# Performance work log

Measured on AMD Instinct MI355X. Metric: run time of the kernel, lower is better.

The kernel has to match this reference:

```python
import jax, jax.numpy as jnp
import numpy as np
import math

P, DD, N, E, NDRUGS = 256, 128, 1024, 250000, 200000
BASELINE = 6.0

def _prelu(x, a):
    return jnp.where(x >= 0, x, a * x)

def _lrelu(x):
    return jnp.where(x >= 0, x, 0.2 * x)

def _lin(x, W, b):
    return x @ W.T + b

def setup_inputs() -> dict:
    key = jax.random.key(0)
    ks = jax.random.split(key, 40)
    f32 = jnp.float32
    inp = {}
    inp["target_features"] = jax.random.normal(ks[0], (P,), f32)
    inp["form_features"] = jax.random.normal(ks[1], (N, P), f32)
    inp["role_features"] = jax.random.normal(ks[2], (N, P), f32)
    inp["form_neighbors"] = jnp.arange(N, dtype=jnp.int32)
    inp["form_binds_src"] = jax.random.randint(ks[3], (E,), 0, N, jnp.int32)
    inp["form_binds_dst"] = jax.random.randint(ks[4], (E,), 0, NDRUGS, jnp.int32)
    inp["form_binds_y"] = jax.random.uniform(ks[5], (E,), f32, 4.0, 9.0)
    inp["role_neighbors"] = jnp.arange(N, dtype=jnp.int32)
    inp["role_binds_src"] = jax.random.randint(ks[6], (E,), 0, N, jnp.int32)
    inp["role_binds_dst"] = jax.random.randint(ks[7], (E,), 0, NDRUGS, jnp.int32)
    inp["role_binds_y"] = jax.random.uniform(ks[8], (E,), f32, 4.0, 9.0)
    inp["drug_features"] = jax.random.normal(ks[9], (NDRUGS, DD), f32)
    s = 0.02
    # prot_refiner: Linear(P,P) -> PReLU -> Linear(P,P)
    inp["Wr1"] = jax.random.normal(ks[10], (P, P), f32) * s
    inp["br1"] = jnp.zeros((P,), f32)
    inp["ar1"] = jnp.asarray(0.25, f32)
    inp["Wr2"] = jax.random.normal(ks[11], (P, P), f32) * s
    inp["br2"] = jnp.zeros((P,), f32)
    # q/k/v projections
    inp["Wq"] = jax.random.normal(ks[12], (DD, P), f32) * s
    inp["bq"] = jnp.zeros((DD,), f32)
    inp["Wk"] = jax.random.normal(ks[13], (DD, DD), f32) * s
    inp["bk"] = jnp.zeros((DD,), f32)
    inp["Wv"] = jax.random.normal(ks[14], (DD, DD), f32) * s
    inp["bv"] = jnp.zeros((DD,), f32)
    inp["layer_emb"] = jax.random.normal(ks[15], (2, 16), f32) * s
    # attn_net: (2P+16)->128->64->1 with LeakyReLU(0.2)
    inp["Wa1"] = jax.random.normal(ks[16], (128, 2 * P + 16), f32) * s
    inp["ba1"] = jnp.zeros((128,), f32)
    inp["Wa2"] = jax.random.normal(ks[17], (64, 128), f32) * s
    inp["ba2"] = jnp.zeros((64,), f32)
    inp["Wa3"] = jax.random.normal(ks[18], (1, 64), f32) * s
    inp["ba3"] = jnp.zeros((1,), f32)
    # integration_mlp: Linear(DD,P) -> PReLU -> Linear(P,P)
    inp["Wi1"] = jax.random.normal(ks[19], (P, DD), f32) * s
    inp["bi1"] = jnp.zeros((P,), f32)
    inp["ai"] = jnp.asarray(0.25, f32)
    inp["Wi2"] = jax.random.normal(ks[20], (P, P), f32) * s
    inp["bi2"] = jnp.zeros((P,), f32)
    inp["ln_g"] = jnp.ones((P,), f32)
    inp["ln_b"] = jnp.zeros((P,), f32)
    return inp

def reference(target_features, form_features, role_features, form_neighbors,
              form_binds_src, form_binds_dst, form_binds_y,
              role_neighbors, role_binds_src, role_binds_dst, role_binds_y,
              drug_features,
              Wr1, br1, ar1, Wr2, br2, Wq, bq, Wk, bk, Wv, bv, layer_emb,
              Wa1, ba1, Wa2, ba2, Wa3, ba3, Wi1, bi1, ai, Wi2, bi2, ln_g, ln_b):
    def refine(x):
        return _lin(_prelu(_lin(x, Wr1, br1), ar1), Wr2, br2)

    zt = refine(target_features)          # [P]
    zf = refine(form_features)            # [N, P]
    zr = refine(role_features)            # [N, P]
    Qv = _lin(zt, Wq, bq)                 # [DD]

    def build_msgs(neighbors, src, dst, y):
        # segment id for each edge: position of src in (sorted) neighbor_ids;
        # edges whose src is not a neighbor go to the dummy segment n.
        n = neighbors.shape[0]
        pos = jnp.clip(jnp.searchsorted(neighbors, src), 0, n - 1)
        seg = jnp.where(neighbors[pos] == src, pos, n)
        d = drug_features[dst]                                # [E, DD] gather
        K = _lin(d, Wk, bk)                                   # [E, DD]
        V = _lin(d, Wv, bv) * (y - BASELINE)[:, None]         # [E, DD]
        s = (K @ Qv) / math.sqrt(DD)                          # [E]
        nseg = n + 1
        m = jax.ops.segment_max(s, seg, num_segments=nseg)    # per-neighbor max
        ex = jnp.exp(s - m[seg])                              # stable softmax numerator
        den = jax.ops.segment_sum(ex, seg, num_segments=nseg)[:n]          # [N]
        num = jax.ops.segment_sum(ex[:, None] * V, seg, num_segments=nseg)[:n]  # [N, DD]
        return jnp.where(den[:, None] > 0, num / jnp.maximum(den, 1e-30)[:, None], 0.0)

    form_msgs = build_msgs(form_neighbors, form_binds_src, form_binds_dst, form_binds_y)
    role_msgs = build_msgs(role_neighbors, role_binds_src, role_binds_dst, role_binds_y)

    def attn(zn, layer_id):
        n = zn.shape[0]
        le = jnp.broadcast_to(layer_emb[layer_id], (n, 16))
        zt_e = jnp.broadcast_to(zt, (n, P))
        x = jnp.concatenate([zt_e, zn, le], axis=-1)          # [N, 2P+16]
        h = _lrelu(_lin(x, Wa1, ba1))
        h = _lrelu(_lin(h, Wa2, ba2))
        return _lin(h, Wa3, ba3)                              # [N, 1]

    all_msgs = jnp.concatenate([form_msgs, role_msgs], axis=0)   # [2N, DD]
    all_attn = jnp.concatenate([attn(zf, 0), attn(zr, 1)], axis=0)  # [2N, 1]
    w = jax.nn.softmax(all_attn, axis=0)
    v_prior = jnp.sum(w * all_msgs, axis=0)                   # [DD]
    integ = _lin(_prelu(_lin(v_prior, Wi1, bi1), ai), Wi2, bi2)
    x = zt + integ
    mu = jnp.mean(x, axis=-1, keepdims=True)
    var = jnp.var(x, axis=-1, keepdims=True)
    z = (x - mu) / jnp.sqrt(var + 1e-5) * ln_g + ln_b
    return (z, form_msgs, role_msgs)
```

## Files before the change

kernel.cpp:

```cpp
#include <hip/hip_runtime.h>

#define NP 256
#define NDD 128
#define NN 1024
#define NE 250000
#define SB 62
#define RB2 257

__global__ __launch_bounds__(256) void prep_kernel(
    const float* __restrict__ Wr1, const float* __restrict__ Wr2,
    const float* __restrict__ Wa1, const float* __restrict__ Wa2,
    const float* __restrict__ Wv,
    float* __restrict__ Wr1T, float* __restrict__ Wr2T,
    float* __restrict__ Wa1mT, float* __restrict__ Wa2T, float* __restrict__ WvT)
{
  __shared__ float T[64][65];
  int b = blockIdx.x, t = threadIdx.x;
  const float* src; float* dst;
  int sC, sr0, sc0, dC, dr0, dc0;
  if (b < 16){        int ti=b;    src=Wr1; sC=256; sr0=(ti/4)*64; sc0=(ti%4)*64;
                      dst=Wr1T; dC=256; dr0=sc0; dc0=sr0; }
  else if (b < 32){   int ti=b-16; src=Wr2; sC=256; sr0=(ti/4)*64; sc0=(ti%4)*64;
                      dst=Wr2T; dC=256; dr0=sc0; dc0=sr0; }
  else if (b < 40){   int ti=b-32; src=Wa1; sC=528; sr0=(ti/4)*64; sc0=256+(ti%4)*64;
                      dst=Wa1mT; dC=128; dr0=(ti%4)*64; dc0=sr0; }
  else if (b < 42){   int ti=b-40; src=Wa2; sC=128; sr0=0; sc0=ti*64;
                      dst=Wa2T; dC=64; dr0=sc0; dc0=0; }
  else {              int ti=b-42; src=Wv;  sC=128; sr0=(ti/2)*64; sc0=(ti%2)*64;
                      dst=WvT; dC=128; dr0=sc0; dc0=sr0; }
  #pragma unroll
  for (int j = 0; j < 16; j++){
    int idx = t + j*256;
    int r = idx >> 6, c = idx & 63;
    T[c][r] = src[(size_t)(sr0 + r)*sC + sc0 + c];
  }
  __syncthreads();
  #pragma unroll
  for (int j = 0; j < 16; j++){
    int idx = t + j*256;
    int r = idx >> 6, c = idx & 63;
    dst[(size_t)(dr0 + r)*dC + dc0 + c] = T[r][c];
  }
}

__global__ __launch_bounds__(256) void refine_qk_hist_kernel(
    const float* __restrict__ tgt, const float* __restrict__ formf, const float* __restrict__ rolef,
    const float* __restrict__ Wr1T, const float* __restrict__ br1, const float* __restrict__ ar1,
    const float* __restrict__ Wr2T, const float* __restrict__ br2,
    const float* __restrict__ Wq, const float* __restrict__ bq,
    const float* __restrict__ Wk, const float* __restrict__ bk,
    const float* __restrict__ Wa1, const float* __restrict__ ba1, const float* __restrict__ lemb,
    const int* __restrict__ neighF, const int* __restrict__ srcF,
    const int* __restrict__ neighR, const int* __restrict__ srcR,
    float* __restrict__ zt, float* __restrict__ zf, float* __restrict__ zr,
    float* __restrict__ qk, float* __restrict__ s0, float* __restrict__ cl,
    int* __restrict__ count)
{
  __shared__ float X[8][NP];
  __shared__ float H[8][NP];
  __shared__ float Zs[NP];
  __shared__ float Q[NDD];
  __shared__ float red[NDD];
  const int t = threadIdx.x;

  if (blockIdx.x >= RB2){
    int bi = blockIdx.x - RB2;
    int role = bi >= SB ? 1 : 0;
    int blk = bi - role*SB;
    const int* neigh = role ? neighR : neighF;
    const int* src   = role ? srcR   : srcF;
    int* cnt = count + role*NN;
    int* NB = (int*)&X[0][0];
    int* lh = NB + NN;
    #pragma unroll
    for (int i = 0; i < NN/256; i++){
      NB[t + i*256] = neigh[t + i*256];
      lh[t + i*256] = 0;
    }
    __syncthreads();
    #pragma unroll
    for (int i = 0; i < 16; i++){
      int e = blk*4096 + i*256 + t;
      if (e < NE){
        int s = src[e];
        int pos;
        if ((unsigned)s < NN && NB[s] == s) pos = s;
        else {
          int lo = 0, hi = NN;
          while (lo < hi){ int mid = (lo+hi)>>1; if (NB[mid] < s) lo = mid+1; else hi = mid; }
          pos = lo < NN ? lo : NN-1;
        }
        if (NB[pos] == s) atomicAdd(&lh[pos], 1);
      }
    }
    __syncthreads();
    #pragma unroll
    for (int i = 0; i < NN/256; i++){
      int c = lh[t + i*256];
      if (c > 0) atomicAdd(&cnt[t + i*256], c);
    }
    return;
  }

  const int base = blockIdx.x * 8;
  #pragma unroll
  for (int r = 0; r < 8; r++){
    int row = base + r;
    if (row < 2*NN + 1){
      const float* xp;
      if (row == 0)        xp = tgt;
      else if (row <= NN)  xp = formf + (size_t)(row-1)*NP;
      else                 xp = rolef + (size_t)(row-NN-1)*NP;
      X[r][t] = xp[t];
    } else {
      X[r][t] = 0.f;
    }
  }
  __syncthreads();
  const float a1 = ar1[0];
  float acc[8];
  #pragma unroll
  for (int r = 0; r < 8; r++) acc[r] = 0.f;
  for (int k = 0; k < NP; k += 4){
    float w0 = Wr1T[(k+0)*NP + t];
    float w1 = Wr1T[(k+1)*NP + t];
    float w2 = Wr1T[(k+2)*NP + t];
    float w3 = Wr1T[(k+3)*NP + t];
    #pragma unroll
    for (int r = 0; r < 8; r++){
      float4 x = *reinterpret_cast<const float4*>(&X[r][k]);
      acc[r] = fmaf(w0, x.x, acc[r]);
      acc[r] = fmaf(w1, x.y, acc[r]);
      acc[r] = fmaf(w2, x.z, acc[r]);
      acc[r] = fmaf(w3, x.w, acc[r]);
    }
  }
  const float b1 = br1[t];
  #pragma unroll
  for (int r = 0; r < 8; r++){
    float h = acc[r] + b1;
    H[r][t] = h >= 0.f ? h : a1*h;
  }
  __syncthreads();
  #pragma unroll
  for (int r = 0; r < 8; r++) acc[r] = 0.f;
  for (int k = 0; k < NP; k += 4){
    float w0 = Wr2T[(k+0)*NP + t];
    float w1 = Wr2T[(k+1)*NP + t];
    float w2 = Wr2T[(k+2)*NP + t];
    float w3 = Wr2T[(k+3)*NP + t];
    #pragma unroll
    for (int r = 0; r < 8; r++){
      float4 h4 = *reinterpret_cast<const float4*>(&H[r][k]);
      acc[r] = fmaf(w0, h4.x, acc[r]);
      acc[r] = fmaf(w1, h4.y, acc[r]);
      acc[r] = fmaf(w2, h4.z, acc[r]);
      acc[r] = fmaf(w3, h4.w, acc[r]);
    }
  }
  const float b2 = br2[t];
  #pragma unroll
  for (int r = 0; r < 8; r++){
    int row = base + r;
    if (row < 2*NN + 1){
      float v = acc[r] + b2;
      float* op;
      if (row == 0){ op = zt; Zs[t] = v; }
      else if (row <= NN)  op = zf + (size_t)(row-1)*NP;
      else                 op = zr + (size_t)(row-NN-1)*NP;
      op[t] = v;
    }
  }

  if (blockIdx.x == 0){
    __syncthreads();
    if (t < NDD){
      float a = 0.f;
      const float4* wq = reinterpret_cast<const float4*>(Wq) + t*(NP/4);
      for (int k4 = 0; k4 < NP/4; k4++){
        float4 w = wq[k4];
        float4 zv = *reinterpret_cast<const float4*>(&Zs[k4*4]);
        a = fmaf(w.x, zv.x, fmaf(w.y, zv.y, fmaf(w.z, zv.z, fmaf(w.w, zv.w, a))));
      }
      float qv = a + bq[t];
      Q[t] = qv;
      red[t] = bk[t] * qv;
    }
    __syncthreads();
    const float rs = 0.08838834764831845f;
    if (t < NDD){
      float a2 = 0.f;
      for (int j = 0; j < NDD; j++) a2 = fmaf(Wk[j*NDD + t], Q[j], a2);
      qk[t] = a2 * rs;
    }
    for (int o = 64; o; o >>= 1){
      if (t < o) red[t] += red[t+o];
      __syncthreads();
    }
    if (t == 0) s0[0] = red[0] * rs;
    {
      int l = t >> 7, tt = t & 127;
      const float4* wrow = reinterpret_cast<const float4*>(Wa1 + (size_t)tt*528);
      float a = 0.f;
      for (int k4 = 0; k4 < 64; k4++){
        float4 w = wrow[k4];
        float4 zv = *reinterpret_cast<const float4*>(&Zs[k4*4]);
        a = fmaf(w.x, zv.x, fmaf(w.y, zv.y, fmaf(w.z, zv.z, fmaf(w.w, zv.w, a))));
      }
      const float* wle = Wa1 + (size_t)tt*528 + 512;
      const float* le = lemb + l*16;
      #pragma unroll
      for (int j = 0; j < 16; j++) a = fmaf(wle[j], le[j], a);
      cl[l*NDD + tt] = a + ba1[tt];
    }
  }
}

__device__ __forceinline__ int seg_of(const int* NB, int s){
  if ((unsigned)s < NN && NB[s] == s) return s;
  int lo = 0, hi = NN;
  while (lo < hi){ int mid = (lo+hi)>>1; if (NB[mid] < s) lo = mid+1; else hi = mid; }
  return lo < NN ? lo : NN-1;
}

__global__ __launch_bounds__(1024) void scatter_kernel(
    const int* __restrict__ neighF, const int* __restrict__ srcF,
    const int* __restrict__ dstF, const float* __restrict__ yF,
    const int* __restrict__ neighR, const int* __restrict__ srcR,
    const int* __restrict__ dstR, const float* __restrict__ yR,
    const int* __restrict__ count, int* __restrict__ cursor0,
    int* __restrict__ offsets, int2* __restrict__ edges)
{
  __shared__ int NB[NN];
  __shared__ int lcur[NN];
  __shared__ int sscan[NN];
  __shared__ int obase[NN];
  __shared__ int lbase[NN];
  int bi = blockIdx.x;
  int role = bi >= SB ? 1 : 0;
  int blk = bi - role*SB;
  const int* neigh = role ? neighR : neighF;
  const int* src   = role ? srcR   : srcF;
  const int* dst   = role ? dstR   : dstF;
  const float* yb  = role ? yR     : yF;
  int* cur0 = cursor0 + role*NN;
  int2* ed  = edges   + (size_t)role*NE;
  int t = threadIdx.x;
  NB[t] = neigh[t];
  lcur[t] = 0;
  int c0 = count[role*NN + t];
  sscan[t] = c0;
  __syncthreads();
  for (int o = 1; o < NN; o <<= 1){
    int v = (t >= o) ? sscan[t-o] : 0;
    __syncthreads();
    sscan[t] += v;
    __syncthreads();
  }
  obase[t] = sscan[t] - c0;
  if (blk == 0) offsets[role*NN + t] = sscan[t] - c0;
  __syncthreads();

  int segr[4], locr[4]; int2 edr[4];
  #pragma unroll
  for (int i = 0; i < 4; i++){
    int e = blk*4096 + i*1024 + t;
    segr[i] = -1;
    if (e < NE){
      int s = src[e];
      int pos = seg_of(NB, s);
      if (NB[pos] == s){
        segr[i] = pos;
        edr[i]  = make_int2(dst[e], __float_as_int(yb[e]));
        locr[i] = atomicAdd(&lcur[pos], 1);
      }
    }
  }
  __syncthreads();
  int c = lcur[t];
  if (c > 0) lbase[t] = obase[t] + atomicAdd(&cur0[t], c);
  __syncthreads();
  #pragma unroll
  for (int i = 0; i < 4; i++){
    if (segr[i] >= 0){
      ed[(size_t)(lbase[segr[i]] + locr[i])] = edr[i];
    }
  }
}

__global__ __launch_bounds__(256) void seg_kernel(
    const float* __restrict__ drug,
    const int2* __restrict__ edges,
    const int* __restrict__ offsets, const int* __restrict__ count,
    const float* __restrict__ qk, const float* __restrict__ s0p,
    float* __restrict__ g, float* __restrict__ den, float* __restrict__ cfac)
{
  int b = blockIdx.x;
  int tid = threadIdx.x;
  int w = tid >> 6, lane = tid & 63, l32 = lane & 31, half = lane >> 5;
  int off = offsets[b], cnt = count[b];
  int l = b >> 10;
  const int2* eb = edges + (size_t)l*NE;
  float4 q = reinterpret_cast<const float4*>(qk)[l32];
  float s0 = s0p[0];
  int chunk = (cnt + 3) >> 2;
  int start = w*chunk;
  int end = min(start + chunk, cnt);
  float dn = 0.f, cc = 0.f;
  float4 ga = make_float4(0.f,0.f,0.f,0.f);
  for (int i = start; i < end; i += 8){
    int dstp[4]; float yp[4]; bool vp[4];
    #pragma unroll
    for (int p2 = 0; p2 < 4; p2++){
      int idx = i + 2*p2 + half;
      bool v = idx < end;
      int2 e = eb[off + (v ? idx : start)];
      dstp[p2] = e.x; yp[p2] = __int_as_float(e.y); vp[p2] = v;
    }
    float4 dv[4];
    #pragma unroll
    for (int p2 = 0; p2 < 4; p2++){
      dv[p2] = reinterpret_cast<const float4*>(drug + (size_t)dstp[p2]*NDD)[l32];
    }
    #pragma unroll
    for (int p2 = 0; p2 < 4; p2++){
      float4 d = dv[p2];
      float s = fmaf(d.x, q.x, fmaf(d.y, q.y, fmaf(d.z, q.z, d.w*q.w)));
      s += __shfl_xor(s, 16, 64);
      s += __shfl_xor(s,  8, 64);
      s += __shfl_xor(s,  4, 64);
      s += __shfl_xor(s,  2, 64);
      s += __shfl_xor(s,  1, 64);
      float ex = vp[p2] ? __expf(s + s0) : 0.f;
      float wv = ex * (yp[p2] - 6.0f);
      dn += ex; cc += wv;
      ga.x = fmaf(wv, d.x, ga.x);
      ga.y = fmaf(wv, d.y, ga.y);
      ga.z = fmaf(wv, d.z, ga.z);
      ga.w = fmaf(wv, d.w, ga.w);
    }
  }
  __shared__ float4 sG[8][32];
  __shared__ float sD[8], sC[8];
  int slot = w*2 + half;
  sG[slot][l32] = ga;
  if (l32 == 0){ sD[slot] = dn; sC[slot] = cc; }
  __syncthreads();
  if (tid < NDD){
    int a = tid >> 2, c = tid & 3;
    float v = 0.f;
    #pragma unroll
    for (int k = 0; k < 8; k++)
      v += reinterpret_cast<const float*>(&sG[k][a])[c];
    g[(size_t)b*NDD + tid] = v;
    if (tid == 0){
      float ds = 0.f, cs = 0.f;
      #pragma unroll
      for (int k = 0; k < 8; k++){ ds += sD[k]; cs += sC[k]; }
      den[b] = ds; cfac[b] = cs;
    }
  }
}

__global__ __launch_bounds__(256) void attn_msgs_kernel(
    const float* __restrict__ zf, const float* __restrict__ zr,
    const float* __restrict__ cl,
    const float* __restrict__ Wa1mT,
    const float* __restrict__ Wa2T, const float* __restrict__ ba2,
    const float* __restrict__ Wa3, const float* __restrict__ ba3,
    const float* __restrict__ g, const float* __restrict__ den, const float* __restrict__ cfac,
    const float* __restrict__ WvT, const float* __restrict__ bv,
    float* __restrict__ attn, float* __restrict__ msgsf, float* __restrict__ outm)
{
  int t = threadIdx.x;
  int tt = t & 127, grp = t >> 7;
  if (blockIdx.x < 256){
    __shared__ float Zn[8][NP];
    __shared__ float H1[8][NDD];
    int base = blockIdx.x*8;
    int layer = blockIdx.x >> 7;
    const float* zsrc = layer ? zr : zf;
    #pragma unroll
    for (int r = 0; r < 8; r++){
      int nn = (base + r) & (NN-1);
      Zn[r][t] = zsrc[(size_t)nn*NP + t];
    }
    __syncthreads();
    float acc[4];
    #pragma unroll
    for (int r = 0; r < 4; r++) acc[r] = 0.f;
    for (int k = 0; k < NP; k += 4){
      float w0 = Wa1mT[(k+0)*NDD + tt];
      float w1 = Wa1mT[(k+1)*NDD + tt];
      float w2 = Wa1mT[(k+2)*NDD + tt];
      float w3 = Wa1mT[(k+3)*NDD + tt];
      #pragma unroll
      for (int r = 0; r < 4; r++){
        float4 x = *reinterpret_cast<const float4*>(&Zn[grp*4 + r][k]);
        acc[r] = fmaf(w0, x.x, acc[r]);
        acc[r] = fmaf(w1, x.y, acc[r]);
        acc[r] = fmaf(w2, x.z, acc[r]);
        acc[r] = fmaf(w3, x.w, acc[r]);
      }
    }
    float c1 = cl[layer*NDD + tt];
    #pragma unroll
    for (int r = 0; r < 4; r++){
      float h = acc[r] + c1;
      H1[grp*4 + r][tt] = h >= 0.f ? h : 0.2f*h;
    }
    __syncthreads();
    if (t < 64){
      float acc2[8];
      #pragma unroll
      for (int r = 0; r < 8; r++) acc2[r] = 0.f;
      for (int k = 0; k < NDD; k += 4){
        float w0 = Wa2T[(k+0)*64 + t];
        float w1 = Wa2T[(k+1)*64 + t];
        float w2 = Wa2T[(k+2)*64 + t];
        float w3 = Wa2T[(k+3)*64 + t];
        #pragma unroll
        for (int r = 0; r < 8; r++){
          float4 h4 = *reinterpret_cast<const float4*>(&H1[r][k]);
          acc2[r] = fmaf(w0, h4.x, acc2[r]);
          acc2[r] = fmaf(w1, h4.y, acc2[r]);
          acc2[r] = fmaf(w2, h4.z, acc2[r]);
          acc2[r] = fmaf(w3, h4.w, acc2[r]);
        }
      }
      float b2 = ba2[t];
      float w3v = Wa3[t];
      float b3 = ba3[0];
      #pragma unroll
      for (int r = 0; r < 8; r++){
        float h = acc2[r] + b2;
        h = h >= 0.f ? h : 0.2f*h;
        float p = w3v * h;
        #pragma unroll
        for (int o = 32; o; o >>= 1) p += __shfl_xor(p, o, 64);
        if (t == 0) attn[base + r] = p + b3;
      }
    }
  } else {
    __shared__ float G[8][NDD];
    int base = (blockIdx.x - 256)*8;
    #pragma unroll
    for (int r = 0; r < 4; r++) G[grp*4 + r][tt] = g[(size_t)(base + grp*4 + r)*NDD + tt];
    __syncthreads();
    float acc[4];
    #pragma unroll
    for (int r = 0; r < 4; r++) acc[r] = 0.f;
    for (int k = 0; k < NDD; k += 4){
      float w0 = WvT[(k+0)*NDD + tt];
      float w1 = WvT[(k+1)*NDD + tt];
      float w2 = WvT[(k+2)*NDD + tt];
      float w3 = WvT[(k+3)*NDD + tt];
      #pragma unroll
      for (int r = 0; r < 4; r++){
        float4 gv = *reinterpret_cast<const float4*>(&G[grp*4 + r][k]);
        acc[r] = fmaf(w0, gv.x, acc[r]);
        acc[r] = fmaf(w1, gv.y, acc[r]);
        acc[r] = fmaf(w2, gv.z, acc[r]);
        acc[r] = fmaf(w3, gv.w, acc[r]);
      }
    }
    float bvj = bv[tt];
    #pragma unroll
    for (int r = 0; r < 4; r++){
      int row = base + grp*4 + r;
      float dn = den[row];
      float v = 0.f;
      if (dn > 0.f) v = (acc[r] + bvj*cfac[row]) / fmaxf(dn, 1e-30f);
      msgsf[(size_t)row*NDD + tt] = v;
      outm [(size_t)row*NDD + tt] = v;
    }
  }
}

__global__ __launch_bounds__(1024) void vprior_final_kernel(
    const float* __restrict__ attn, const float* __restrict__ msgsf,
    const float* __restrict__ zt,
    const float* __restrict__ Wi1, const float* __restrict__ bi1, const float* __restrict__ ai,
    const float* __restrict__ Wi2, const float* __restrict__ bi2,
    const float* __restrict__ ln_g, const float* __restrict__ ln_b,
    float* __restrict__ zout)
{
  __shared__ float A[2*NN];
  __shared__ float red[1024];
  __shared__ float Pp[8][NDD];
  __shared__ float V[NDD];
  __shared__ float T1[NP];
  __shared__ float red2[NP];
  int t = threadIdx.x;
  A[t] = attn[t]; A[t+1024] = attn[t+1024];
  __syncthreads();
  float mx = fmaxf(A[t], A[t+1024]);
  red[t] = mx; __syncthreads();
  for (int o = 512; o; o >>= 1){ if (t < o) red[t] = fmaxf(red[t], red[t+o]); __syncthreads(); }
  float M = red[0]; __syncthreads();
  float sm = __expf(A[t] - M) + __expf(A[t+1024] - M);
  red[t] = sm; __syncthreads();
  for (int o = 512; o; o >>= 1){ if (t < o) red[t] += red[t+o]; __syncthreads(); }
  float inv = 1.f / red[0]; __syncthreads();
  A[t]      = __expf(A[t]      - M) * inv;
  A[t+1024] = __expf(A[t+1024] - M) * inv;
  __syncthreads();
  int j = t & 127, grp = t >> 7;
  float acc = 0.f;
  int i0 = grp * 256;
  for (int i = i0; i < i0 + 256; i++) acc = fmaf(A[i], msgsf[(size_t)i*NDD + j], acc);
  Pp[grp][j] = acc;
  __syncthreads();
  if (t < NDD){
    float v = 0.f;
    #pragma unroll
    for (int gg = 0; gg < 8; gg++) v += Pp[gg][t];
    V[t] = v;
  }
  __syncthreads();
  float x = 0.f;
  if (t < NP){
    float a1 = 0.f;
    const float4* w1 = reinterpret_cast<const float4*>(Wi1) + t*(NDD/4);
    for (int k4 = 0; k4 < NDD/4; k4++){
      float4 w = w1[k4];
      float4 vv = *reinterpret_cast<const float4*>(&V[k4*4]);
      a1 = fmaf(w.x, vv.x, fmaf(w.y, vv.y, fmaf(w.z, vv.z, fmaf(w.w, vv.w, a1))));
    }
    float h = a1 + bi1[t];
    float a = ai[0];
    T1[t] = h >= 0.f ? h : a*h;
  }
  __syncthreads();
  if (t < NP){
    float a2 = 0.f;
    const float4* w2 = reinterpret_cast<const float4*>(Wi2) + t*(NP/4);
    for (int k4 = 0; k4 < NP/4; k4++){
      float4 w = w2[k4];
      float4 hv = *reinterpret_cast<const float4*>(&T1[k4*4]);
      a2 = fmaf(w.x, hv.x, fmaf(w.y, hv.y, fmaf(w.z, hv.z, fmaf(w.w, hv.w, a2))));
    }
    x = zt[t] + a2 + bi2[t];
    red2[t] = x;
  }
  __syncthreads();
  for (int o = 128; o; o >>= 1){ if (t < o) red2[t] += red2[t+o]; __syncthreads(); }
  float mu = red2[0] * (1.f/256.f); __syncthreads();
  float d = x - mu;
  if (t < NP) red2[t] = d*d;
  __syncthreads();
  for (int o = 128; o; o >>= 1){ if (t < o) red2[t] += red2[t+o]; __syncthreads(); }
  if (t < NP){
    float var = red2[0] * (1.f/256.f);
    float zz = d * rsqrtf(var + 1e-5f) * ln_g[t] + ln_b[t];
    zout[t] = zz;
  }
}

extern "C" void kernel_launch(void* const* d_in, const int* in_sizes, int n_in,
                              void* d_out, int out_size, void* d_ws, size_t ws_size,
                              hipStream_t stream)
{
  const float* tgt    = (const float*)d_in[0];
  const float* formf  = (const float*)d_in[1];
  const float* rolef  = (const float*)d_in[2];
  const int* fneigh   = (const int*)d_in[3];
  const int* fsrc     = (const int*)d_in[4];
  const int* fdst     = (const int*)d_in[5];
  const float* fy     = (const float*)d_in[6];
  const int* rneigh   = (const int*)d_in[7];
  const int* rsrc     = (const int*)d_in[8];
  const int* rdst     = (const int*)d_in[9];
  const float* ry     = (const float*)d_in[10];
  const float* drug   = (const float*)d_in[11];
  const float* Wr1 = (const float*)d_in[12];
  const float* br1 = (const float*)d_in[13];
  const float* ar1 = (const float*)d_in[14];
  const float* Wr2 = (const float*)d_in[15];
  const float* br2 = (const float*)d_in[16];
  const float* Wq  = (const float*)d_in[17];
  const float* bq  = (const float*)d_in[18];
  const float* Wk  = (const float*)d_in[19];
  const float* bk  = (const float*)d_in[20];
  const float* Wv  = (const float*)d_in[21];
  const float* bv  = (const float*)d_in[22];
  const float* lemb= (const float*)d_in[23];
  const float* Wa1 = (const float*)d_in[24];
  const float* ba1 = (const float*)d_in[25];
  const float* Wa2 = (const float*)d_in[26];
  const float* ba2 = (const float*)d_in[27];
  const float* Wa3 = (const float*)d_in[28];
  const float* ba3 = (const float*)d_in[29];
  const float* Wi1 = (const float*)d_in[30];
  const float* bi1 = (const float*)d_in[31];
  const float* ai  = (const float*)d_in[32];
  const float* Wi2 = (const float*)d_in[33];
  const float* bi2 = (const float*)d_in[34];
  const float* lng = (const float*)d_in[35];
  const float* lnb = (const float*)d_in[36];
  (void)in_sizes; (void)n_in; (void)out_size; (void)ws_size;

  float* ws = (float*)d_ws;
  float* zt_     = ws + 0;
  float* zf_     = ws + 256;
  float* zr_     = ws + 262400;
  float* qk_     = ws + 524544;
  float* s0_     = ws + 524672;
  float* cl_     = ws + 524800;
  float* attn_   = ws + 525056;
  float* den_    = ws + 527104;
  float* cfac_   = ws + 529152;
  float* g_      = ws + 531200;
  float* msgsf_  = ws + 793344;
  int*   count_  = (int*)(ws + 1055488);
  int*   offs_   = (int*)(ws + 1057536);
  int*   cursor_ = (int*)(ws + 1059584);
  int2*  edges_  = (int2*)(ws + 1061632);
  float* Wr1T_   = ws + 3061632;
  float* Wr2T_   = ws + 3127168;
  float* Wa1mT_  = ws + 3192704;
  float* Wa2T_   = ws + 3225472;
  float* WvT_    = ws + 3233664;

  hipMemsetAsync(count_, 0, 3*2*NN*sizeof(int), stream);

  prep_kernel<<<46, 256, 0, stream>>>(Wr1, Wr2, Wa1, Wa2, Wv,
                                      Wr1T_, Wr2T_, Wa1mT_, Wa2T_, WvT_);

  refine_qk_hist_kernel<<<RB2 + 2*SB, 256, 0, stream>>>(
      tgt, formf, rolef, Wr1T_, br1, ar1, Wr2T_, br2, Wq, bq, Wk, bk,
      Wa1, ba1, lemb,
      fneigh, fsrc, rneigh, rsrc,
      zt_, zf_, zr_, qk_, s0_, cl_, count_);

  scatter_kernel<<<2*SB, 1024, 0, stream>>>(fneigh, fsrc, fdst, fy,
                                            rneigh, rsrc, rdst, ry,
                                            count_, cursor_, offs_, edges_);

  seg_kernel<<<2*NN, 256, 0, stream>>>(drug, edges_, offs_, count_, qk_, s0_,
                                       g_, den_, cfac_);

  attn_msgs_kernel<<<512, 256, 0, stream>>>(zf_, zr_, cl_,
                                            Wa1mT_, Wa2T_, ba2, Wa3, ba3,
                                            g_, den_, cfac_, WvT_, bv,
                                            attn_, msgsf_, (float*)d_out + NP);
  vprior_final_kernel<<<1, 1024, 0, stream>>>(attn_, msgsf_, zt_,
                                              Wi1, bi1, ai, Wi2, bi2,
                                              lng, lnb, (float*)d_out);
}
```

Measured before the change: 367.4 us.

## Fuse attention MLP into refine kernel and Wv projection into segment kernel

Moves the target-row refine and the q/k/cl computation into an extra block of the prep kernel. The neighbor refine kernel now runs the attention MLP straight on its refined rows, so zf/zr never go to global memory. The Wv projection is folded into the segment kernel, which drops the g/den/cfac round trip and removes the attn_msgs kernel launch. In exchange the refine blocks do more serial work and each segment block runs a small per-row matvec, and launch bounds of 4 waves/SIMD are added that may limit registers.

```diff
diff --git a/kernel.cpp b/kernel.cpp
--- a/kernel.cpp
+++ b/kernel.cpp
@@ -5,17 +5,95 @@
 #define NN 1024
 #define NE 250000
 #define SB 62
-#define RB2 257
+#define RB 256
 
 __global__ __launch_bounds__(256) void prep_kernel(
     const float* __restrict__ Wr1, const float* __restrict__ Wr2,
     const float* __restrict__ Wa1, const float* __restrict__ Wa2,
     const float* __restrict__ Wv,
+    const float* __restrict__ tgt, const float* __restrict__ br1,
+    const float* __restrict__ ar1, const float* __restrict__ br2,
+    const float* __restrict__ Wq, const float* __restrict__ bq,
+    const float* __restrict__ Wk, const float* __restrict__ bk,
+    const float* __restrict__ ba1, const float* __restrict__ lemb,
     float* __restrict__ Wr1T, float* __restrict__ Wr2T,
-    float* __restrict__ Wa1mT, float* __restrict__ Wa2T, float* __restrict__ WvT)
+    float* __restrict__ Wa1mT, float* __restrict__ Wa2T, float* __restrict__ WvT,
+    float* __restrict__ zt, float* __restrict__ qk, float* __restrict__ s0,
+    float* __restrict__ cl)
 {
+  int b = blockIdx.x, t = threadIdx.x;
+  if (b == 46){
+    __shared__ float Xs[NP], Hs[NP], Zs[NP], Q[NDD], red[NDD];
+    Xs[t] = tgt[t];
+    __syncthreads();
+    float a = 0.f;
+    {
+      const float4* w1 = reinterpret_cast<const float4*>(Wr1) + (size_t)t*(NP/4);
+      for (int k4 = 0; k4 < NP/4; k4++){
+        float4 w = w1[k4];
+        float4 x = *reinterpret_cast<const float4*>(&Xs[k4*4]);
+        a = fmaf(w.x,x.x,fmaf(w.y,x.y,fmaf(w.z,x.z,fmaf(w.w,x.w,a))));
+      }
+    }
+    float h = a + br1[t];
+    float a1 = ar1[0];
+    Hs[t] = h >= 0.f ? h : a1*h;
+    __syncthreads();
+    a = 0.f;
+    {
+      const float4* w2 = reinterpret_cast<const float4*>(Wr2) + (size_t)t*(NP/4);
+      for (int k4 = 0; k4 < NP/4; k4++){
+        float4 w = w2[k4];
+        float4 x = *reinterpret_cast<const float4*>(&Hs[k4*4]);
+        a = fmaf(w.x,x.x,fmaf(w.y,x.y,fmaf(w.z,x.z,fmaf(w.w,x.w,a))));
+      }
+    }
+    float zv = a + br2[t];
+    Zs[t] = zv;
+    zt[t] = zv;
+    __syncthreads();
+    if (t < NDD){
+      float aq = 0.f;
+      const float4* wq = reinterpret_cast<const float4*>(Wq) + (size_t)t*(NP/4);
+      for (int k4 = 0; k4 < NP/4; k4++){
+        float4 w = wq[k4];
+        float4 x = *reinterpret_cast<const float4*>(&Zs[k4*4]);
+        aq = fmaf(w.x,x.x,fmaf(w.y,x.y,fmaf(w.z,x.z,fmaf(w.w,x.w,aq))));
+      }
+      float qv = aq + bq[t];
+      Q[t] = qv;
+      red[t] = bk[t]*qv;
+    }
+    __syncthreads();
+    const float rs = 0.08838834764831845f;
+    if (t < NDD){
+      float a2 = 0.f;
+      for (int j = 0; j < NDD; j++) a2 = fmaf(Wk[j*NDD + t], Q[j], a2);
+      qk[t] = a2 * rs;
+    }
+    for (int o = 64; o; o >>= 1){
+      if (t < o) red[t] += red[t+o];
+      __syncthreads();
+    }
+    if (t == 0) s0[0] = red[0]*rs;
+    {
+      int l = t >> 7, tt = t & 127;
+      const float4* wrow = reinterpret_cast<const float4*>(Wa1 + (size_t)tt*528);
+      float ac = 0.f;
+      for (int k4 = 0; k4 < 64; k4++){
+        float4 w = wrow[k4];
+        float4 x = *reinterpret_cast<const float4*>(&Zs[k4*4]);
+        ac = fmaf(w.x,x.x,fmaf(w.y,x.y,fmaf(w.z,x.z,fmaf(w.w,x.w,ac))));
+      }
+      const float* wle = Wa1 + (size_t)tt*528 + 512;
+      const float* le = lemb + l*16;
+      #pragma unroll
+      for (int j2 = 0; j2 < 16; j2++) ac = fmaf(wle[j2], le[j2], ac);
+      cl[l*NDD + tt] = ac + ba1[tt];
+    }
+    return;
+  }
   __shared__ float T[64][65];
-  int b = blockIdx.x, t = threadIdx.x;
   const float* src; float* dst;
   int sC, sr0, sc0, dC, dr0, dc0;
   if (b < 16){        int ti=b;    src=Wr1; sC=256; sr0=(ti/4)*64; sc0=(ti%4)*64;
@@ -43,28 +121,24 @@
   }
 }
 
-__global__ __launch_bounds__(256) void refine_qk_hist_kernel(
-    const float* __restrict__ tgt, const float* __restrict__ formf, const float* __restrict__ rolef,
+__global__ __launch_bounds__(256, 4) void refine_attn_hist_kernel(
+    const float* __restrict__ formf, const float* __restrict__ rolef,
     const float* __restrict__ Wr1T, const float* __restrict__ br1, const float* __restrict__ ar1,
     const float* __restrict__ Wr2T, const float* __restrict__ br2,
-    const float* __restrict__ Wq, const float* __restrict__ bq,
-    const float* __restrict__ Wk, const float* __restrict__ bk,
-    const float* __restrict__ Wa1, const float* __restrict__ ba1, const float* __restrict__ lemb,
+    const float* __restrict__ cl, const float* __restrict__ Wa1mT,
+    const float* __restrict__ Wa2T, const float* __restrict__ ba2,
+    const float* __restrict__ Wa3, const float* __restrict__ ba3,
     const int* __restrict__ neighF, const int* __restrict__ srcF,
     const int* __restrict__ neighR, const int* __restrict__ srcR,
-    float* __restrict__ zt, float* __restrict__ zf, float* __restrict__ zr,
-    float* __restrict__ qk, float* __restrict__ s0, float* __restrict__ cl,
-    int* __restrict__ count)
+    float* __restrict__ attn, int* __restrict__ count)
 {
   __shared__ float X[8][NP];
   __shared__ float H[8][NP];
-  __shared__ float Zs[NP];
-  __shared__ float Q[NDD];
-  __shared__ float red[NDD];
+  __shared__ float H1[8][NDD];
   const int t = threadIdx.x;
 
-  if (blockIdx.x >= RB2){
-    int bi = blockIdx.x - RB2;
+  if (blockIdx.x >= RB){
+    int bi = blockIdx.x - RB;
     int role = bi >= SB ? 1 : 0;
     int blk = bi - role*SB;
     const int* neigh = role ? neighR : neighF;
@@ -102,19 +176,13 @@
     return;
   }
 
-  const int base = blockIdx.x * 8;
+  const int abase = blockIdx.x * 8;
+  const int layer = blockIdx.x >> 7;
+  const float* fsrcp = layer ? rolef : formf;
   #pragma unroll
   for (int r = 0; r < 8; r++){
-    int row = base + r;
-    if (row < 2*NN + 1){
-      const float* xp;
-      if (row == 0)        xp = tgt;
-      else if (row <= NN)  xp = formf + (size_t)(row-1)*NP;
-      else                 xp = rolef + (size_t)(row-NN-1)*NP;
-      X[r][t] = xp[t];
-    } else {
-      X[r][t] = 0.f;
-    }
+    int nn = (abase + r) & (NN-1);
+    X[r][t] = fsrcp[(size_t)nn*NP + t];
   }
   __syncthreads();
   const float a1 = ar1[0];
@@ -160,58 +228,63 @@
   }
   const float b2 = br2[t];
   #pragma unroll
-  for (int r = 0; r < 8; r++){
-    int row = base + r;
-    if (row < 2*NN + 1){
-      float v = acc[r] + b2;
-      float* op;
-      if (row == 0){ op = zt; Zs[t] = v; }
-      else if (row <= NN)  op = zf + (size_t)(row-1)*NP;
-      else                 op = zr + (size_t)(row-NN-1)*NP;
-      op[t] = v;
-    }
-  }
-
-  if (blockIdx.x == 0){
-    __syncthreads();
-    if (t < NDD){
-      float a = 0.f;
-      const float4* wq = reinterpret_cast<const float4*>(Wq) + t*(NP/4);
-      for (int k4 = 0; k4 < NP/4; k4++){
-        float4 w = wq[k4];
-        float4 zv = *reinterpret_cast<const float4*>(&Zs[k4*4]);
-        a = fmaf(w.x, zv.x, fmaf(w.y, zv.y, fmaf(w.z, zv.z, fmaf(w.w, zv.w, a))));
+  for (int r = 0; r < 8; r++) X[r][t] = acc[r] + b2;
+  __syncthreads();
+
+  const int tt = t & 127, grp = t >> 7;
+  const float c1 = cl[layer*NDD + tt];
+  float acc2[4];
+  #pragma unroll
+  for (int r = 0; r < 4; r++) acc2[r] = 0.f;
+  for (int k = 0; k < NP; k += 4){
+    float w0 = Wa1mT[(k+0)*NDD + tt];
+    float w1 = Wa1mT[(k+1)*NDD + tt];
+    float w2 = Wa1mT[(k+2)*NDD + tt];
+    float w3 = Wa1mT[(k+3)*NDD + tt];
+    #pragma unroll
+    for (int r = 0; r < 4; r++){
+      float4 x = *reinterpret_cast<const float4*>(&X[grp*4 + r][k]);
+      acc2[r] = fmaf(w0, x.x, acc2[r]);
+      acc2[r] = fmaf(w1, x.y, acc2[r]);
+      acc2[r] = fmaf(w2, x.z, acc2[r]);
+      acc2[r] = fmaf(w3, x.w, acc2[r]);
+    }
+  }
+  #pragma unroll
+  for (int r = 0; r < 4; r++){
+    float h = acc2[r] + c1;
+    H1[grp*4 + r][tt] = h >= 0.f ? h : 0.2f*h;
+  }
+  __syncthreads();
+  if (t < 64){
+    float a2r[8];
+    #pragma unroll
+    for (int r = 0; r < 8; r++) a2r[r] = 0.f;
+    for (int k = 0; k < NDD; k += 4){
+      float w0 = Wa2T[(k+0)*64 + t];
+      float w1 = Wa2T[(k+1)*64 + t];
+      float w2 = Wa2T[(k+2)*64 + t];
+      float w3 = Wa2T[(k+3)*64 + t];
+      #pragma unroll
+      for (int r = 0; r < 8; r++){
+        float4 h4 = *reinterpret_cast<const float4*>(&H1[r][k]);
+        a2r[r] = fmaf(w0, h4.x, a2r[r]);
+        a2r[r] = fmaf(w1, h4.y, a2r[r]);
+        a2r[r] = fmaf(w2, h4.z, a2r[r]);
+        a2r[r] = fmaf(w3, h4.w, a2r[r]);
       }
-      float qv = a + bq[t];
-      Q[t] = qv;
-      red[t] = bk[t] * qv;
-    }
-    __syncthreads();
-    const float rs = 0.08838834764831845f;
-    if (t < NDD){
-      float a2 = 0.f;
-      for (int j = 0; j < NDD; j++) a2 = fmaf(Wk[j*NDD + t], Q[j], a2);
-      qk[t] = a2 * rs;
-    }
-    for (int o = 64; o; o >>= 1){
-      if (t < o) red[t] += red[t+o];
-      __syncthreads();
-    }
-    if (t == 0) s0[0] = red[0] * rs;
-    {
-      int l = t >> 7, tt = t & 127;
-      const float4* wrow = reinterpret_cast<const float4*>(Wa1 + (size_t)tt*528);
-      float a = 0.f;
-      for (int k4 = 0; k4 < 64; k4++){
-        float4 w = wrow[k4];
-        float4 zv = *reinterpret_cast<const float4*>(&Zs[k4*4]);
-        a = fmaf(w.x, zv.x, fmaf(w.y, zv.y, fmaf(w.z, zv.z, fmaf(w.w, zv.w, a))));
-      }
-      const float* wle = Wa1 + (size_t)tt*528 + 512;
-      const float* le = lemb + l*16;
+    }
+    float b2a = ba2[t];
+    float w3v = Wa3[t];
+    float b3 = ba3[0];
+    #pragma unroll
+    for (int r = 0; r < 8; r++){
+      float h = a2r[r] + b2a;
+      h = h >= 0.f ? h : 0.2f*h;
+      float p = w3v * h;
       #pragma unroll
-      for (int j = 0; j < 16; j++) a = fmaf(wle[j], le[j], a);
-      cl[l*NDD + tt] = a + ba1[tt];
+      for (int o = 32; o; o >>= 1) p += __shfl_xor(p, o, 64);
+      if (t == 0) attn[abase + r] = p + b3;
     }
   }
 }
@@ -288,12 +361,13 @@
   }
 }
 
-__global__ __launch_bounds__(256) void seg_kernel(
+__global__ __launch_bounds__(256, 4) void seg_msgs_kernel(
     const float* __restrict__ drug,
     const int2* __restrict__ edges,
     const int* __restrict__ offsets, const int* __restrict__ count,
     const float* __restrict__ qk, const float* __restrict__ s0p,
-    float* __restrict__ g, float* __restrict__ den, float* __restrict__ cfac)
+    const float* __restrict__ WvT, const float* __restrict__ bv,
+    float* __restrict__ msgsf, float* __restrict__ outm)
 {
   int b = blockIdx.x;
   int tid = threadIdx.x;
@@ -342,6 +416,9 @@
   }
   __shared__ float4 sG[8][32];
   __shared__ float sD[8], sC[8];
+  __shared__ float Grow[NDD];
+  __shared__ float part[2][NDD];
+  __shared__ float sDen, sCfac;
   int slot = w*2 + half;
   sG[slot][l32] = ga;
   if (l32 == 0){ sD[slot] = dn; sC[slot] = cc; }
@@ -352,128 +429,35 @@
     #pragma unroll
     for (int k = 0; k < 8; k++)
       v += reinterpret_cast<const float*>(&sG[k][a])[c];
-    g[(size_t)b*NDD + tid] = v;
+    Grow[tid] = v;
     if (tid == 0){
       float ds = 0.f, cs = 0.f;
       #pragma unroll
       for (int k = 0; k < 8; k++){ ds += sD[k]; cs += sC[k]; }
-      den[b] = ds; cfac[b] = cs;
-    }
-  }
-}
-
-__global__ __launch_bounds__(256) void attn_msgs_kernel(
-    const float* __restrict__ zf, const float* __restrict__ zr,
-    const float* __restrict__ cl,
-    const float* __restrict__ Wa1mT,
-    const float* __restrict__ Wa2T, const float* __restrict__ ba2,
-    const float* __restrict__ Wa3, const float* __restrict__ ba3,
-    const float* __restrict__ g, const float* __restrict__ den, const float* __restrict__ cfac,
-    const float* __restrict__ WvT, const float* __restrict__ bv,
-    float* __restrict__ attn, float* __restrict__ msgsf, float* __restrict__ outm)
-{
-  int t = threadIdx.x;
-  int tt = t & 127, grp = t >> 7;
-  if (blockIdx.x < 256){
-    __shared__ float Zn[8][NP];
-    __shared__ float H1[8][NDD];
-    int base = blockIdx.x*8;
-    int layer = blockIdx.x >> 7;
-    const float* zsrc = layer ? zr : zf;
-    #pragma unroll
-    for (int r = 0; r < 8; r++){
-      int nn = (base + r) & (NN-1);
-      Zn[r][t] = zsrc[(size_t)nn*NP + t];
-    }
-    __syncthreads();
-    float acc[4];
-    #pragma unroll
-    for (int r = 0; r < 4; r++) acc[r] = 0.f;
-    for (int k = 0; k < NP; k += 4){
-      float w0 = Wa1mT[(k+0)*NDD + tt];
-      float w1 = Wa1mT[(k+1)*NDD + tt];
-      float w2 = Wa1mT[(k+2)*NDD + tt];
-      float w3 = Wa1mT[(k+3)*NDD + tt];
-      #pragma unroll
-      for (int r = 0; r < 4; r++){
-        float4 x = *reinterpret_cast<const float4*>(&Zn[grp*4 + r][k]);
-        acc[r] = fmaf(w0, x.x, acc[r]);
-        acc[r] = fmaf(w1, x.y, acc[r]);
-        acc[r] = fmaf(w2, x.z, acc[r]);
-        acc[r] = fmaf(w3, x.w, acc[r]);
-      }
-    }
-    float c1 = cl[layer*NDD + tt];
-    #pragma unroll
-    for (int r = 0; r < 4; r++){
-      float h = acc[r] + c1;
-      H1[grp*4 + r][tt] = h >= 0.f ? h : 0.2f*h;
-    }
-    __syncthreads();
-    if (t < 64){
-      float acc2[8];
-      #pragma unroll
-      for (int r = 0; r < 8; r++) acc2[r] = 0.f;
-      for (int k = 0; k < NDD; k += 4){
-        float w0 = Wa2T[(k+0)*64 + t];
-        float w1 = Wa2T[(k+1)*64 + t];
-        float w2 = Wa2T[(k+2)*64 + t];
-        float w3 = Wa2T[(k+3)*64 + t];
-        #pragma unroll
-        for (int r = 0; r < 8; r++){
-          float4 h4 = *reinterpret_cast<const float4*>(&H1[r][k]);
-          acc2[r] = fmaf(w0, h4.x, acc2[r]);
-          acc2[r] = fmaf(w1, h4.y, acc2[r]);
-          acc2[r] = fmaf(w2, h4.z, acc2[r]);
-          acc2[r] = fmaf(w3, h4.w, acc2[r]);
-        }
-      }
-      float b2 = ba2[t];
-      float w3v = Wa3[t];
-      float b3 = ba3[0];
-      #pragma unroll
-      for (int r = 0; r < 8; r++){
-        float h = acc2[r] + b2;
-        h = h >= 0.f ? h : 0.2f*h;
-        float p = w3v * h;
-        #pragma unroll
-        for (int o = 32; o; o >>= 1) p += __shfl_xor(p, o, 64);
-        if (t == 0) attn[base + r] = p + b3;
-      }
-    }
-  } else {
-    __shared__ float G[8][NDD];
-    int base = (blockIdx.x - 256)*8;
-    #pragma unroll
-    for (int r = 0; r < 4; r++) G[grp*4 + r][tt] = g[(size_t)(base + grp*4 + r)*NDD + tt];
-    __syncthreads();
-    float acc[4];
-    #pragma unroll
-    for (int r = 0; r < 4; r++) acc[r] = 0.f;
-    for (int k = 0; k < NDD; k += 4){
+      sDen = ds; sCfac = cs;
+    }
+  }
+  __syncthreads();
+  {
+    int tt = tid & 127, grp = tid >> 7;
+    float acc = 0.f;
+    for (int k = grp*64; k < grp*64 + 64; k += 4){
       float w0 = WvT[(k+0)*NDD + tt];
       float w1 = WvT[(k+1)*NDD + tt];
       float w2 = WvT[(k+2)*NDD + tt];
       float w3 = WvT[(k+3)*NDD + tt];
-      #pragma unroll
-      for (int r = 0; r < 4; r++){
-        float4 gv = *reinterpret_cast<const float4*>(&G[grp*4 + r][k]);
-        acc[r] = fmaf(w0, gv.x, acc[r]);
-        acc[r] = fmaf(w1, gv.y, acc[r]);
-        acc[r] = fmaf(w2, gv.z, acc[r]);
-        acc[r] = fmaf(w3, gv.w, acc[r]);
-      }
-    }
-    float bvj = bv[tt];
-    #pragma unroll
-    for (int r = 0; r < 4; r++){
-      int row = base + grp*4 + r;
-      float dn = den[row];
-      float v = 0.f;
-      if (dn > 0.f) v = (acc[r] + bvj*cfac[row]) / fmaxf(dn, 1e-30f);
-      msgsf[(size_t)row*NDD + tt] = v;
-      outm [(size_t)row*NDD + tt] = v;
-    }
+      float4 gv = *reinterpret_cast<const float4*>(&Grow[k]);
+      acc = fmaf(w0, gv.x, fmaf(w1, gv.y, fmaf(w2, gv.z, fmaf(w3, gv.w, acc))));
+    }
+    part[grp][tt] = acc;
+  }
+  __syncthreads();
+  if (tid < NDD){
+    float dnm = sDen;
+    float v = 0.f;
+    if (dnm > 0.f) v = (part[0][tid] + part[1][tid] + bv[tid]*sCfac) / fmaxf(dnm, 1e-30f);
+    msgsf[(size_t)b*NDD + tid] = v;
+    outm [(size_t)b*NDD + tid] = v;
   }
 }
 
@@ -602,15 +586,10 @@
 
   float* ws = (float*)d_ws;
   float* zt_     = ws + 0;
-  float* zf_     = ws + 256;
-  float* zr_     = ws + 262400;
   float* qk_     = ws + 524544;
   float* s0_     = ws + 524672;
   float* cl_     = ws + 524800;
   float* attn_   = ws + 525056;
-  float* den_    = ws + 527104;
-  float* cfac_   = ws + 529152;
-  float* g_      = ws + 531200;
   float* msgsf_  = ws + 793344;
   int*   count_  = (int*)(ws + 1055488);
   int*   offs_   = (int*)(ws + 1057536);
@@ -624,26 +603,25 @@
 
   hipMemsetAsync(count_, 0, 3*2*NN*sizeof(int), stream);
 
-  prep_kernel<<<46, 256, 0, stream>>>(Wr1, Wr2, Wa1, Wa2, Wv,
-                                      Wr1T_, Wr2T_, Wa1mT_, Wa2T_, WvT_);
-
-  refine_qk_hist_kernel<<<RB2 + 2*SB, 256, 0, stream>>>(
-      tgt, formf, rolef, Wr1T_, br1, ar1, Wr2T_, br2, Wq, bq, Wk, bk,
-      Wa1, ba1, lemb,
+  prep_kernel<<<47, 256, 0, stream>>>(Wr1, Wr2, Wa1, Wa2, Wv,
+                                      tgt, br1, ar1, br2, Wq, bq, Wk, bk, ba1, lemb,
+                                      Wr1T_, Wr2T_, Wa1mT_, Wa2T_, WvT_,
+                                      zt_, qk_, s0_, cl_);
+
+  refine_attn_hist_kernel<<<RB + 2*SB, 256, 0, stream>>>(
+      formf, rolef, Wr1T_, br1, ar1, Wr2T_, br2,
+      cl_, Wa1mT_, Wa2T_, ba2, Wa3, ba3,
       fneigh, fsrc, rneigh, rsrc,
-      zt_, zf_, zr_, qk_, s0_, cl_, count_);
+      attn_, count_);
 
   scatter_kernel<<<2*SB, 1024, 0, stream>>>(fneigh, fsrc, fdst, fy,
                                             rneigh, rsrc, rdst, ry,
                                             count_, cursor_, offs_, edges_);
 
-  seg_kernel<<<2*NN, 256, 0, stream>>>(drug, edges_, offs_, count_, qk_, s0_,
-                                       g_, den_, cfac_);
-
-  attn_msgs_kernel<<<512, 256, 0, stream>>>(zf_, zr_, cl_,
-                                            Wa1mT_, Wa2T_, ba2, Wa3, ba3,
-                                            g_, den_, cfac_, WvT_, bv,
-                                            attn_, msgsf_, (float*)d_out + NP);
+  seg_msgs_kernel<<<2*NN, 256, 0, stream>>>(drug, edges_, offs_, count_, qk_, s0_,
+                                            WvT_, bv,
+                                            msgsf_, (float*)d_out + NP);
+
   vprior_final_kernel<<<1, 1024, 0, stream>>>(attn_, msgsf_, zt_,
                                               Wi1, bi1, ai, Wi2, bi2,
                                               lng, lnb, (float*)d_out);
```

New measurement: 365.1 us. About the same (-0.6%).
